# Kernel optimization log

Hardware: AMD Instinct MI355X
Metric: run time of the kernel (lower is better)

The kernel has to match this reference:

```python
import jax, jax.numpy as jnp
import numpy as np
from jax import lax

EPS = 1e-5

def _dsconv(x, dw, pw, g, b, m, v, relu):
    # x: [B,C,H,W]; dw: [C,1,3,3] depthwise; pw: [C,C,1,1] pointwise; eval-mode BN
    C = x.shape[1]
    y = lax.conv_general_dilated(x, dw, (1, 1), 'SAME', feature_group_count=C)
    y = lax.conv_general_dilated(y, pw, (1, 1), 'SAME')
    scale = (g * lax.rsqrt(v + EPS))[None, :, None, None]
    y = y * scale + (b - m * g * lax.rsqrt(v + EPS))[None, :, None, None]
    return jnp.maximum(y, 0.0) if relu else y

def _attention(x, wq, bq, wk, bk, wv, bv, gamma):
    b, c, h, w = x.shape
    n = h * w
    xf = x.reshape(b, c, n)                      # [B,C,N]
    q = jnp.einsum('oc,bcn->bon', wq, xf) + bq[None, :, None]   # [B,C/8,N]
    k = jnp.einsum('oc,bcn->bon', wk, xf) + bk[None, :, None]   # [B,C/8,N]
    v = jnp.einsum('oc,bcn->bon', wv, xf) + bv[None, :, None]   # [B,C,N]
    logits = jnp.einsum('bdm,bdn->bmn', q, k)    # q^T k, [B,N,N]
    attn = jax.nn.softmax(logits, axis=2)
    out = jnp.einsum('bcn,bmn->bcm', v, attn).reshape(b, c, h, w)
    return gamma[0] * out + x

def setup_inputs() -> dict:
    key = jax.random.key(0)
    ks = jax.random.split(key, 20)
    B, C, H, W = 64, 256, 32, 32
    C8 = C // 8
    rn = lambda k, s, sc: (jax.random.normal(k, s, dtype=jnp.float32) * sc)
    return {
        'x': rn(ks[0], (B, C, H, W), 1.0),
        'dw1': rn(ks[1], (C, 1, 3, 3), 0.2),
        'pw1': rn(ks[2], (C, C, 1, 1), 0.06),
        'bn1_g': jax.random.uniform(ks[3], (C,), jnp.float32, 0.5, 1.5),
        'bn1_b': rn(ks[4], (C,), 0.1),
        'bn1_m': rn(ks[5], (C,), 0.1),
        'bn1_v': jax.random.uniform(ks[6], (C,), jnp.float32, 0.5, 1.5),
        'dw2': rn(ks[7], (C, 1, 3, 3), 0.2),
        'pw2': rn(ks[8], (C, C, 1, 1), 0.06),
        'bn2_g': jax.random.uniform(ks[9], (C,), jnp.float32, 0.5, 1.5),
        'bn2_b': rn(ks[10], (C,), 0.1),
        'bn2_m': rn(ks[11], (C,), 0.1),
        'bn2_v': jax.random.uniform(ks[12], (C,), jnp.float32, 0.5, 1.5),
        'wq': rn(ks[13], (C8, C), 0.06),
        'bq': rn(ks[14], (C8,), 0.02),
        'wk': rn(ks[15], (C8, C), 0.06),
        'bk': rn(ks[16], (C8,), 0.02),
        'wv': rn(ks[17], (C, C), 0.06),
        'bv': rn(ks[18], (C,), 0.02),
        'gamma': rn(ks[19], (1,), 0.5),
    }

def reference(x, dw1, pw1, bn1_g, bn1_b, bn1_m, bn1_v,
              dw2, pw2, bn2_g, bn2_b, bn2_m, bn2_v,
              wq, bq, wk, bk, wv, bv, gamma):
    out = _dsconv(x, dw1, pw1, bn1_g, bn1_b, bn1_m, bn1_v, relu=True)
    out = _dsconv(out, dw2, pw2, bn2_g, bn2_b, bn2_m, bn2_v, relu=False)
    out = _attention(out + x, wq, bq, wk, bk, wv, bv, gamma)
    return jnp.maximum(out, 0.0)
```

## Files before the change

kernel.cpp:

```cpp
#include <hip/hip_runtime.h>
#include <cstdint>
#include <cstddef>

#define B_ 64
#define C_ 256
#define N_ 1024

typedef short v8s __attribute__((ext_vector_type(8)));
typedef float v4f __attribute__((ext_vector_type(4)));
typedef unsigned int u32;
typedef unsigned short u16;

__device__ __forceinline__ float bf2f(u16 u) {
  return __uint_as_float(((u32)u) << 16);
}
__device__ __forceinline__ u16 f2bf(float f) {
  u32 x = __float_as_uint(f);
  x += 0x7fffu + ((x >> 16) & 1u);
  return (u16)(x >> 16);
}
__device__ __forceinline__ u32 pack2(float a, float b) {
  return (u32)f2bf(a) | ((u32)f2bf(b) << 16);
}

typedef __attribute__((address_space(3))) unsigned int lds_as_t;
typedef __attribute__((address_space(1))) const unsigned int glb_as_t;
__device__ __forceinline__ void ld_lds16(const u16* g, u16* l) {
  __builtin_amdgcn_global_load_lds((glb_as_t*)g, (lds_as_t*)l, 16, 0, 0);
}

__global__ __launch_bounds__(256) void prep(
    const float* __restrict__ g1, const float* __restrict__ b1,
    const float* __restrict__ m1, const float* __restrict__ v1,
    const float* __restrict__ g2, const float* __restrict__ b2,
    const float* __restrict__ m2, const float* __restrict__ v2,
    const float* __restrict__ wq, const float* __restrict__ bq,
    const float* __restrict__ wk, const float* __restrict__ bk,
    const float* __restrict__ wv, const float* __restrict__ bv,
    const float* __restrict__ pw1, const float* __restrict__ pw2,
    const float* __restrict__ dw1, const float* __restrict__ dw2,
    float* __restrict__ scale1, float* __restrict__ shift1,
    float* __restrict__ scale2, float* __restrict__ shift2,
    float* __restrict__ dwT1, float* __restrict__ dwT2,
    u16* __restrict__ pw1b, u16* __restrict__ pw2b, u16* __restrict__ wcatb,
    float* __restrict__ bcat) {
  const int gt = blockIdx.x * 256 + threadIdx.x;
  if (gt < 256) {
    float s1 = g1[gt] * rsqrtf(v1[gt] + 1e-5f);
    scale1[gt] = s1;
    shift1[gt] = b1[gt] - m1[gt] * s1;
    float s2 = g2[gt] * rsqrtf(v2[gt] + 1e-5f);
    scale2[gt] = s2;
    shift2[gt] = b2[gt] - m2[gt] * s2;
  }
  if (gt < 320) bcat[gt] = (gt < 32) ? bq[gt] : (gt < 64) ? bk[gt - 32] : bv[gt - 64];
  if (gt < 2304) {
    dwT1[(gt % 9) * 256 + gt / 9] = dw1[gt];
    dwT2[(gt % 9) * 256 + gt / 9] = dw2[gt];
  }
  for (int e = gt; e < 65536; e += 16384) {
    pw1b[e] = f2bf(pw1[e]);
    pw2b[e] = f2bf(pw2[e]);
  }
  for (int e = gt; e < 81920; e += 16384) {
    const int o = e >> 8;
    float w = (o < 32) ? wq[e] : (o < 64) ? wk[e - 8192] : wv[e - 16384];
    wcatb[e] = f2bf(w);
  }
}

__global__ __launch_bounds__(256) void transpose_x(const float* __restrict__ x,
                                                   u16* __restrict__ xt) {
  __shared__ float t[64][65];
  const int b = blockIdx.z, c0 = blockIdx.y * 64, n0 = blockIdx.x * 64;
  const float* xp = x + ((size_t)b * C_ + c0) * N_ + n0;
  const int tn = threadIdx.x & 63, tc = threadIdx.x >> 6;
#pragma unroll
  for (int i = 0; i < 16; ++i)
    t[tc + 4 * i][tn] = xp[(size_t)(tc + 4 * i) * N_ + tn];
  __syncthreads();
  u16* op = xt + ((size_t)b * N_ + n0) * C_ + c0;
  const int oc = threadIdx.x & 63, on = threadIdx.x >> 6;
#pragma unroll
  for (int i = 0; i < 16; ++i)
    op[(size_t)(on + 4 * i) * C_ + oc] = f2bf(t[oc][on + 4 * i]);
}

__global__ __launch_bounds__(256) void dw_nhwc(const u16* __restrict__ src,
                                               const float* __restrict__ wT,
                                               u16* __restrict__ dst) {
  __shared__ float wl[9][256];
  const int b = blockIdx.y;
  for (int e = threadIdx.x; e < 2304; e += 256) wl[e >> 8][e & 255] = wT[e];
  __syncthreads();
  const int pl = threadIdx.x >> 5, c0 = (threadIdx.x & 31) * 8;
  const int p = blockIdx.x * 8 + pl;
  const int h = p >> 5, wx = p & 31;
  const u16* sp = src + (size_t)b * N_ * C_;
  float acc[8] = {0.f, 0.f, 0.f, 0.f, 0.f, 0.f, 0.f, 0.f};
#pragma unroll
  for (int dh = -1; dh <= 1; ++dh) {
    const int hh = h + dh;
    if (hh < 0 || hh > 31) continue;
#pragma unroll
    for (int dx = -1; dx <= 1; ++dx) {
      const int ww = wx + dx;
      if (ww < 0 || ww > 31) continue;
      const int k = (dh + 1) * 3 + (dx + 1);
      const uint4 v = *(const uint4*)(sp + (size_t)(hh * 32 + ww) * C_ + c0);
      const u32 vv[4] = {v.x, v.y, v.z, v.w};
#pragma unroll
      for (int j = 0; j < 4; ++j) {
        acc[2 * j] += bf2f((u16)(vv[j] & 0xffffu)) * wl[k][c0 + 2 * j];
        acc[2 * j + 1] += bf2f((u16)(vv[j] >> 16)) * wl[k][c0 + 2 * j + 1];
      }
    }
  }
  uint4 o4;
  o4.x = pack2(acc[0], acc[1]);
  o4.y = pack2(acc[2], acc[3]);
  o4.z = pack2(acc[4], acc[5]);
  o4.w = pack2(acc[6], acc[7]);
  *(uint4*)(dst + ((size_t)b * N_ + p) * C_ + c0) = o4;
}

template <int EPI>
__global__ __launch_bounds__(256) void gemm(
    const u16* __restrict__ X, const u16* __restrict__ W,
    const float* __restrict__ scale, const float* __restrict__ shift,
    const u16* __restrict__ resid, u16* __restrict__ Y, u16* __restrict__ Y2) {
  __shared__ u16 Xs[128][64];
  __shared__ u16 Ws[128][64];
  const int tid = threadIdx.x;
  const int b = blockIdx.z;
  const int n0 = blockIdx.x * 128, o0 = blockIdx.y * 128;
  const int wid = tid >> 6, lane = tid & 63;
  const int wn = wid & 1, wo = wid >> 1;
  const int l15 = lane & 15, l4 = lane >> 4;
  const int lr = lane >> 3, lc = (lane & 7) * 8;

  v4f acc[4][4];
#pragma unroll
  for (int i = 0; i < 4; ++i)
#pragma unroll
    for (int j = 0; j < 4; ++j) acc[i][j] = v4f{0.f, 0.f, 0.f, 0.f};

  for (int k0 = 0; k0 < C_; k0 += 64) {
#pragma unroll
    for (int g = 0; g < 4; ++g) {
      const int base = wid * 32 + g * 8;
      const int xr = n0 + base + lr;
      ld_lds16(X + ((size_t)b * N_ + xr) * C_ + k0 + lc, &Xs[base][0]);
      int wr = o0 + base + lr;
      if (EPI == 2 && wr > 319) wr = 319;
      ld_lds16(W + (size_t)wr * C_ + k0 + lc, &Ws[base][0]);
    }
    __syncthreads();
#pragma unroll
    for (int ks = 0; ks < 2; ++ks) {
      v8s af[4], bf4[4];
#pragma unroll
      for (int f = 0; f < 4; ++f) {
        af[f] = *(const v8s*)&Ws[wo * 64 + f * 16 + l15][ks * 32 + l4 * 8];
        bf4[f] = *(const v8s*)&Xs[wn * 64 + f * 16 + l15][ks * 32 + l4 * 8];
      }
#pragma unroll
      for (int i = 0; i < 4; ++i)
#pragma unroll
        for (int j = 0; j < 4; ++j)
          acc[i][j] = __builtin_amdgcn_mfma_f32_16x16x32_bf16(
              af[i], bf4[j], acc[i][j], 0, 0, 0);
    }
    __syncthreads();
  }

#pragma unroll
  for (int i = 0; i < 4; ++i) {
    const int obase = o0 + wo * 64 + i * 16 + l4 * 4;
#pragma unroll
    for (int j = 0; j < 4; ++j) {
      const int n = n0 + wn * 64 + j * 16 + l15;
      float y0 = acc[i][j][0], y1 = acc[i][j][1];
      float y2 = acc[i][j][2], y3 = acc[i][j][3];
      if constexpr (EPI == 0 || EPI == 1) {
        const float4 sc = *(const float4*)&scale[obase];
        const float4 sh = *(const float4*)&shift[obase];
        y0 = y0 * sc.x + sh.x;
        y1 = y1 * sc.y + sh.y;
        y2 = y2 * sc.z + sh.z;
        y3 = y3 * sc.w + sh.w;
        if constexpr (EPI == 0) {
          y0 = fmaxf(y0, 0.f);
          y1 = fmaxf(y1, 0.f);
          y2 = fmaxf(y2, 0.f);
          y3 = fmaxf(y3, 0.f);
        } else {
          const uint2 rb =
              *(const uint2*)(resid + ((size_t)b * N_ + n) * C_ + obase);
          y0 += bf2f((u16)(rb.x & 0xffffu));
          y1 += bf2f((u16)(rb.x >> 16));
          y2 += bf2f((u16)(rb.y & 0xffffu));
          y3 += bf2f((u16)(rb.y >> 16));
        }
        uint2 st;
        st.x = pack2(y0, y1);
        st.y = pack2(y2, y3);
        *(uint2*)&Y[((size_t)b * N_ + n) * C_ + obase] = st;
      } else {
        if (obase >= 320) continue;
        const float4 bi = *(const float4*)&shift[obase];
        y0 += bi.x;
        y1 += bi.y;
        y2 += bi.z;
        y3 += bi.w;
        if (obase < 64) {
          uint2 st;
          st.x = pack2(y0, y1);
          st.y = pack2(y2, y3);
          *(uint2*)&Y[((size_t)b * N_ + n) * 64 + obase] = st;
        } else {
          const int c = obase - 64;
          Y2[((size_t)b * C_ + c) * N_ + n] = f2bf(y0);
          Y2[((size_t)b * C_ + c + 1) * N_ + n] = f2bf(y1);
          Y2[((size_t)b * C_ + c + 2) * N_ + n] = f2bf(y2);
          Y2[((size_t)b * C_ + c + 3) * N_ + n] = f2bf(y3);
        }
      }
    }
  }
}

__global__ __launch_bounds__(256) void flash(const u16* __restrict__ qk,
                                             const u16* __restrict__ vchw,
                                             const u16* __restrict__ abf,
                                             const float* __restrict__ gamma_p,
                                             float* __restrict__ out) {
  const int b = blockIdx.y;
  const int m0 = blockIdx.x * 64;
  const int tid = threadIdx.x, wid = tid >> 6, lane = tid & 63;
  const int l15 = lane & 15, l4 = lane >> 4;
  const int mw = m0 + wid * 16;

  __shared__ u16 Vs[2][256][64];
  __shared__ u16 Plds[4][16][72];

  const u16* qkb = qk + (size_t)b * N_ * 64;
  const u16* vb = vchw + (size_t)b * C_ * N_;

  const v8s qf = *(const v8s*)&qkb[(size_t)(mw + l15) * 64 + l4 * 8];

  const int src_c = lane >> 3;
  const int src_j = (lane & 7) ^ (lane >> 3);

  v8s kf[4];
#pragma unroll
  for (int g = 0; g < 8; ++g) {
    const int base = wid * 64 + g * 8;
    ld_lds16(vb + (size_t)(base + src_c) * N_ + src_j * 8, &Vs[0][base][0]);
  }
#pragma unroll
  for (int f = 0; f < 4; ++f)
    kf[f] = *(const v8s*)&qkb[(size_t)(f * 16 + l15) * 64 + 32 + l4 * 8];
  __syncthreads();

  float M = -3e38f, S = 0.f;
  v4f acc[16];
#pragma unroll
  for (int i = 0; i < 16; ++i) acc[i] = v4f{0.f, 0.f, 0.f, 0.f};

  for (int t = 0; t < 16; ++t) {
    const int cur = t & 1;
    v4f lt[4];
#pragma unroll
    for (int f = 0; f < 4; ++f)
      lt[f] = __builtin_amdgcn_mfma_f32_16x16x32_bf16(
          kf[f], qf, v4f{0.f, 0.f, 0.f, 0.f}, 0, 0, 0);
    if (t < 15) {
      const int n1 = (t + 1) * 64;
#pragma unroll
      for (int g = 0; g < 8; ++g) {
        const int base = wid * 64 + g * 8;
        ld_lds16(vb + (size_t)(base + src_c) * N_ + n1 + src_j * 8,
                 &Vs[cur ^ 1][base][0]);
      }
#pragma unroll
      for (int f = 0; f < 4; ++f)
        kf[f] = *(const v8s*)&qkb[(size_t)(n1 + f * 16 + l15) * 64 + 32 +
                                  l4 * 8];
    }
    float pmax = -3e38f;
#pragma unroll
    for (int f = 0; f < 4; ++f)
#pragma unroll
      for (int r = 0; r < 4; ++r) pmax = fmaxf(pmax, lt[f][r]);
    pmax = fmaxf(pmax, __shfl_xor(pmax, 16));
    pmax = fmaxf(pmax, __shfl_xor(pmax, 32));
    const float Mnew = fmaxf(M, pmax);
    if (__any(Mnew > M)) {
      const float fsc = __expf(M - Mnew);
      S *= fsc;
      M = Mnew;
      float fr[4];
#pragma unroll
      for (int r = 0; r < 4; ++r) fr[r] = __shfl(fsc, l4 * 4 + r);
#pragma unroll
      for (int cf = 0; cf < 16; ++cf)
#pragma unroll
        for (int r = 0; r < 4; ++r) acc[cf][r] *= fr[r];
    }
    float ssum = 0.f;
#pragma unroll
    for (int f = 0; f < 4; ++f) {
      const float p0 = __expf(lt[f][0] - M);
      const float p1 = __expf(lt[f][1] - M);
      const float p2 = __expf(lt[f][2] - M);
      const float p3 = __expf(lt[f][3] - M);
      ssum += (p0 + p1) + (p2 + p3);
      uint2 pw;
      pw.x = pack2(p0, p1);
      pw.y = pack2(p2, p3);
      *(uint2*)&Plds[wid][l15][f * 16 + l4 * 4] = pw;
    }
    S += ssum;
#pragma unroll
    for (int ks = 0; ks < 2; ++ks) {
      const v8s pa = *(const v8s*)&Plds[wid][l15][ks * 32 + l4 * 8];
#pragma unroll
      for (int cf = 0; cf < 16; ++cf) {
        const int col = 8 * (((ks * 4) + l4) ^ (l15 & 7));
        const v8s vf = *(const v8s*)&Vs[cur][cf * 16 + l15][col];
        acc[cf] = __builtin_amdgcn_mfma_f32_16x16x32_bf16(pa, vf, acc[cf], 0,
                                                          0, 0);
      }
    }
    __syncthreads();
  }

  S += __shfl_xor(S, 16);
  S += __shfl_xor(S, 32);
  const float inv = 1.f / S;
  const float g = gamma_p[0];
  float invr[4];
#pragma unroll
  for (int r = 0; r < 4; ++r) invr[r] = __shfl(inv, l4 * 4 + r);
  const int mb = mw + l4 * 4;
#pragma unroll
  for (int cf = 0; cf < 16; ++cf) {
    const int c = cf * 16 + l15;
    float4 y;
    float* yp = (float*)&y;
#pragma unroll
    for (int r = 0; r < 4; ++r) {
      const float av = bf2f(abf[((size_t)b * N_ + mb + r) * C_ + c]);
      yp[r] = fmaxf(g * acc[cf][r] * invr[r] + av, 0.f);
    }
    *(float4*)&out[((size_t)b * C_ + c) * N_ + mb] = y;
  }
}

extern "C" void kernel_launch(void* const* d_in, const int* in_sizes, int n_in,
                              void* d_out, int out_size, void* d_ws,
                              size_t ws_size, hipStream_t stream) {
  const float* x = (const float*)d_in[0];
  const float* dw1 = (const float*)d_in[1];
  const float* pw1 = (const float*)d_in[2];
  const float* bn1g = (const float*)d_in[3];
  const float* bn1b = (const float*)d_in[4];
  const float* bn1m = (const float*)d_in[5];
  const float* bn1v = (const float*)d_in[6];
  const float* dw2 = (const float*)d_in[7];
  const float* pw2 = (const float*)d_in[8];
  const float* bn2g = (const float*)d_in[9];
  const float* bn2b = (const float*)d_in[10];
  const float* bn2m = (const float*)d_in[11];
  const float* bn2v = (const float*)d_in[12];
  const float* wq = (const float*)d_in[13];
  const float* bq = (const float*)d_in[14];
  const float* wk = (const float*)d_in[15];
  const float* bk = (const float*)d_in[16];
  const float* wv = (const float*)d_in[17];
  const float* bv = (const float*)d_in[18];
  const float* gamma = (const float*)d_in[19];
  float* out = (float*)d_out;

  char* ws = (char*)d_ws;
  size_t off = 0;
  auto alloc = [&](size_t bytes) {
    void* p = ws + off;
    off += (bytes + 255) & ~(size_t)255;
    return p;
  };
  const size_t NE = (size_t)B_ * N_ * C_;

  u16* bufA = (u16*)alloc(NE * 2);
  u16* bufB = (u16*)alloc(NE * 2);
  u16* bufC = (u16*)alloc(NE * 2);
  u16* abf = (u16*)alloc(NE * 2);
  float* scale1 = (float*)alloc(256 * 4);
  float* shift1 = (float*)alloc(256 * 4);
  float* scale2 = (float*)alloc(256 * 4);
  float* shift2 = (float*)alloc(256 * 4);
  float* dwT1 = (float*)alloc(2304 * 4);
  float* dwT2 = (float*)alloc(2304 * 4);
  u16* pw1b = (u16*)alloc(65536 * 2);
  u16* pw2b = (u16*)alloc(65536 * 2);
  u16* wcatb = (u16*)alloc(81920 * 2);
  float* bcat = (float*)alloc(320 * 4);

  u16* xt = bufA;
  u16* t1 = bufB;
  u16* y1 = bufC;
  u16* t2 = bufB;
  u16* qkbuf = bufC;
  u16* vchw = bufA;

  prep<<<64, 256, 0, stream>>>(bn1g, bn1b, bn1m, bn1v, bn2g, bn2b, bn2m, bn2v,
                               wq, bq, wk, bk, wv, bv, pw1, pw2, dw1, dw2,
                               scale1, shift1, scale2, shift2, dwT1, dwT2,
                               pw1b, pw2b, wcatb, bcat);
  transpose_x<<<dim3(16, 4, B_), 256, 0, stream>>>(x, xt);
  dw_nhwc<<<dim3(128, B_), 256, 0, stream>>>(xt, dwT1, t1);
  gemm<0><<<dim3(8, 2, B_), 256, 0, stream>>>(t1, pw1b, scale1, shift1,
                                              nullptr, y1, nullptr);
  dw_nhwc<<<dim3(128, B_), 256, 0, stream>>>(y1, dwT2, t2);
  gemm<1><<<dim3(8, 2, B_), 256, 0, stream>>>(t2, pw2b, scale2, shift2, xt,
                                              abf, nullptr);
  gemm<2><<<dim3(8, 3, B_), 256, 0, stream>>>(abf, wcatb, nullptr, bcat,
                                              nullptr, qkbuf, vchw);
  flash<<<dim3(16, B_), 256, 0, stream>>>(qkbuf, vchw, abf, gamma, out);
}
```

Baseline: 259.6 us.

## Precompute softmax max in a pre-pass, stage GEMM epilogue stores through LDS

```diff
diff --git a/kernel.cpp b/kernel.cpp
--- a/kernel.cpp
+++ b/kernel.cpp
@@ -5,6 +5,7 @@
 #define B_ 64
 #define C_ 256
 #define N_ 1024
+#define LOG2E 1.4426950408889634f
 
 typedef short v8s __attribute__((ext_vector_type(8)));
 typedef float v4f __attribute__((ext_vector_type(4)));
@@ -53,7 +54,9 @@
     scale2[gt] = s2;
     shift2[gt] = b2[gt] - m2[gt] * s2;
   }
-  if (gt < 320) bcat[gt] = (gt < 32) ? bq[gt] : (gt < 64) ? bk[gt - 32] : bv[gt - 64];
+  if (gt < 320)
+    bcat[gt] = (gt < 32) ? bq[gt] * LOG2E
+                         : (gt < 64) ? bk[gt - 32] : bv[gt - 64];
   if (gt < 2304) {
     dwT1[(gt % 9) * 256 + gt / 9] = dw1[gt];
     dwT2[(gt % 9) * 256 + gt / 9] = dw2[gt];
@@ -64,7 +67,8 @@
   }
   for (int e = gt; e < 81920; e += 16384) {
     const int o = e >> 8;
-    float w = (o < 32) ? wq[e] : (o < 64) ? wk[e - 8192] : wv[e - 16384];
+    float w = (o < 32) ? wq[e] * LOG2E
+                       : (o < 64) ? wk[e - 8192] : wv[e - 16384];
     wcatb[e] = f2bf(w);
   }
 }
@@ -129,8 +133,11 @@
     const u16* __restrict__ X, const u16* __restrict__ W,
     const float* __restrict__ scale, const float* __restrict__ shift,
     const u16* __restrict__ resid, u16* __restrict__ Y, u16* __restrict__ Y2) {
-  __shared__ u16 Xs[128][64];
-  __shared__ u16 Ws[128][64];
+  __shared__ u16 smem[17408];
+  u16(*Xs)[64] = (u16(*)[64])smem;
+  u16(*Ws)[64] = (u16(*)[64])(smem + 8192);
+  u16(*Ys)[136] = (u16(*)[136])smem;
+
   const int tid = threadIdx.x;
   const int b = blockIdx.z;
   const int n0 = blockIdx.x * 128, o0 = blockIdx.y * 128;
@@ -149,8 +156,8 @@
 #pragma unroll
     for (int g = 0; g < 4; ++g) {
       const int base = wid * 32 + g * 8;
-      const int xr = n0 + base + lr;
-      ld_lds16(X + ((size_t)b * N_ + xr) * C_ + k0 + lc, &Xs[base][0]);
+      ld_lds16(X + ((size_t)b * N_ + n0 + base + lr) * C_ + k0 + lc,
+               &Xs[base][0]);
       int wr = o0 + base + lr;
       if (EPI == 2 && wr > 319) wr = 319;
       ld_lds16(W + (size_t)wr * C_ + k0 + lc, &Ws[base][0]);
@@ -161,8 +168,13 @@
       v8s af[4], bf4[4];
 #pragma unroll
       for (int f = 0; f < 4; ++f) {
-        af[f] = *(const v8s*)&Ws[wo * 64 + f * 16 + l15][ks * 32 + l4 * 8];
-        bf4[f] = *(const v8s*)&Xs[wn * 64 + f * 16 + l15][ks * 32 + l4 * 8];
+        if constexpr (EPI != 2) {
+          af[f] = *(const v8s*)&Ws[wo * 64 + f * 16 + l15][ks * 32 + l4 * 8];
+          bf4[f] = *(const v8s*)&Xs[wn * 64 + f * 16 + l15][ks * 32 + l4 * 8];
+        } else {
+          af[f] = *(const v8s*)&Xs[wn * 64 + f * 16 + l15][ks * 32 + l4 * 8];
+          bf4[f] = *(const v8s*)&Ws[wo * 64 + f * 16 + l15][ks * 32 + l4 * 8];
+        }
       }
 #pragma unroll
       for (int i = 0; i < 4; ++i)
@@ -174,21 +186,20 @@
     __syncthreads();
   }
 
-#pragma unroll
-  for (int i = 0; i < 4; ++i) {
-    const int obase = o0 + wo * 64 + i * 16 + l4 * 4;
-#pragma unroll
-    for (int j = 0; j < 4; ++j) {
-      const int n = n0 + wn * 64 + j * 16 + l15;
-      float y0 = acc[i][j][0], y1 = acc[i][j][1];
-      float y2 = acc[i][j][2], y3 = acc[i][j][3];
-      if constexpr (EPI == 0 || EPI == 1) {
-        const float4 sc = *(const float4*)&scale[obase];
-        const float4 sh = *(const float4*)&shift[obase];
-        y0 = y0 * sc.x + sh.x;
-        y1 = y1 * sc.y + sh.y;
-        y2 = y2 * sc.z + sh.z;
-        y3 = y3 * sc.w + sh.w;
+  if constexpr (EPI != 2) {
+#pragma unroll
+    for (int i = 0; i < 4; ++i) {
+      const int oL = wo * 64 + i * 16 + l4 * 4;
+      const int o = o0 + oL;
+      const float4 sc = *(const float4*)&scale[o];
+      const float4 sh = *(const float4*)&shift[o];
+#pragma unroll
+      for (int j = 0; j < 4; ++j) {
+        const int nL = wn * 64 + j * 16 + l15;
+        float y0 = acc[i][j][0] * sc.x + sh.x;
+        float y1 = acc[i][j][1] * sc.y + sh.y;
+        float y2 = acc[i][j][2] * sc.z + sh.z;
+        float y3 = acc[i][j][3] * sc.w + sh.w;
         if constexpr (EPI == 0) {
           y0 = fmaxf(y0, 0.f);
           y1 = fmaxf(y1, 0.f);
@@ -196,7 +207,7 @@
           y3 = fmaxf(y3, 0.f);
         } else {
           const uint2 rb =
-              *(const uint2*)(resid + ((size_t)b * N_ + n) * C_ + obase);
+              *(const uint2*)(resid + ((size_t)b * N_ + n0 + nL) * C_ + o);
           y0 += bf2f((u16)(rb.x & 0xffffu));
           y1 += bf2f((u16)(rb.x >> 16));
           y2 += bf2f((u16)(rb.y & 0xffffu));
@@ -205,26 +216,59 @@
         uint2 st;
         st.x = pack2(y0, y1);
         st.y = pack2(y2, y3);
-        *(uint2*)&Y[((size_t)b * N_ + n) * C_ + obase] = st;
-      } else {
-        if (obase >= 320) continue;
-        const float4 bi = *(const float4*)&shift[obase];
-        y0 += bi.x;
-        y1 += bi.y;
-        y2 += bi.z;
-        y3 += bi.w;
-        if (obase < 64) {
+        *(uint2*)&Ys[nL][oL] = st;
+      }
+    }
+    __syncthreads();
+#pragma unroll
+    for (int s = 0; s < 8; ++s) {
+      const int nL = s * 16 + (tid >> 4);
+      const int slot = tid & 15;
+      const uint4 v = *(const uint4*)&Ys[nL][slot * 8];
+      *(uint4*)&Y[((size_t)b * N_ + n0 + nL) * C_ + o0 + slot * 8] = v;
+    }
+  } else {
+    float bj[4];
+#pragma unroll
+    for (int j = 0; j < 4; ++j) {
+      int o = o0 + wo * 64 + j * 16 + l15;
+      bj[j] = shift[o > 319 ? 319 : o];
+    }
+    if (o0 == 0 && wo == 0) {
+#pragma unroll
+      for (int i = 0; i < 4; ++i) {
+        const int nB = n0 + wn * 64 + i * 16 + l4 * 4;
+#pragma unroll
+        for (int j = 0; j < 4; ++j) {
+          const int o = j * 16 + l15;
+#pragma unroll
+          for (int r = 0; r < 4; ++r)
+            Y[((size_t)b * N_ + nB + r) * 64 + o] = f2bf(acc[i][j][r] + bj[j]);
+        }
+      }
+    } else {
+#pragma unroll
+      for (int i = 0; i < 4; ++i) {
+        const int nL = wn * 64 + i * 16 + l4 * 4;
+#pragma unroll
+        for (int j = 0; j < 4; ++j) {
+          const int oL = wo * 64 + j * 16 + l15;
           uint2 st;
-          st.x = pack2(y0, y1);
-          st.y = pack2(y2, y3);
-          *(uint2*)&Y[((size_t)b * N_ + n) * 64 + obase] = st;
-        } else {
-          const int c = obase - 64;
-          Y2[((size_t)b * C_ + c) * N_ + n] = f2bf(y0);
-          Y2[((size_t)b * C_ + c + 1) * N_ + n] = f2bf(y1);
-          Y2[((size_t)b * C_ + c + 2) * N_ + n] = f2bf(y2);
-          Y2[((size_t)b * C_ + c + 3) * N_ + n] = f2bf(y3);
+          st.x = pack2(acc[i][j][0] + bj[j], acc[i][j][1] + bj[j]);
+          st.y = pack2(acc[i][j][2] + bj[j], acc[i][j][3] + bj[j]);
+          *(uint2*)&Ys[oL][nL] = st;
         }
+      }
+    }
+    __syncthreads();
+#pragma unroll
+    for (int s = 0; s < 8; ++s) {
+      const int oL = s * 16 + (tid >> 4);
+      const int c = o0 + oL - 64;
+      if (c >= 0 && c < 256) {
+        const int slot = tid & 15;
+        const uint4 v = *(const uint4*)&Ys[oL][slot * 8];
+        *(uint4*)&Y2[((size_t)b * C_ + c) * N_ + n0 + slot * 8] = v;
       }
     }
   }
@@ -235,8 +279,8 @@
                                              const u16* __restrict__ abf,
                                              const float* __restrict__ gamma_p,
                                              float* __restrict__ out) {
-  const int b = blockIdx.y;
-  const int m0 = blockIdx.x * 64;
+  const int b = blockIdx.x;
+  const int m0 = blockIdx.y * 64;
   const int tid = threadIdx.x, wid = tid >> 6, lane = tid & 63;
   const int l15 = lane & 15, l4 = lane >> 4;
   const int mw = m0 + wid * 16;
@@ -246,27 +290,54 @@
 
   const u16* qkb = qk + (size_t)b * N_ * 64;
   const u16* vb = vchw + (size_t)b * C_ * N_;
-
   const v8s qf = *(const v8s*)&qkb[(size_t)(mw + l15) * 64 + l4 * 8];
 
   const int src_c = lane >> 3;
   const int src_j = (lane & 7) ^ (lane >> 3);
 
-  v8s kf[4];
 #pragma unroll
   for (int g = 0; g < 8; ++g) {
     const int base = wid * 64 + g * 8;
     ld_lds16(vb + (size_t)(base + src_c) * N_ + src_j * 8, &Vs[0][base][0]);
   }
+
+  float Mloc = -3e38f;
+  v8s kf[4];
+#pragma unroll
+  for (int f = 0; f < 4; ++f)
+    kf[f] = *(const v8s*)&qkb[(size_t)(f * 16 + l15) * 64 + 32 + l4 * 8];
+  for (int t = 0; t < 16; ++t) {
+    v8s kn[4];
+    if (t < 15) {
+      const int n1 = (t + 1) * 64;
+#pragma unroll
+      for (int f = 0; f < 4; ++f)
+        kn[f] =
+            *(const v8s*)&qkb[(size_t)(n1 + f * 16 + l15) * 64 + 32 + l4 * 8];
+    }
+#pragma unroll
+    for (int f = 0; f < 4; ++f) {
+      const v4f lt = __builtin_amdgcn_mfma_f32_16x16x32_bf16(
+          kf[f], qf, v4f{0.f, 0.f, 0.f, 0.f}, 0, 0, 0);
+      Mloc = fmaxf(Mloc, fmaxf(fmaxf(lt[0], lt[1]), fmaxf(lt[2], lt[3])));
+    }
+    if (t < 15) {
+#pragma unroll
+      for (int f = 0; f < 4; ++f) kf[f] = kn[f];
+    }
+  }
+  Mloc = fmaxf(Mloc, __shfl_xor(Mloc, 16));
+  Mloc = fmaxf(Mloc, __shfl_xor(Mloc, 32));
+  const float M = Mloc;
+
+  v4f acc[16];
+#pragma unroll
+  for (int i = 0; i < 16; ++i) acc[i] = v4f{0.f, 0.f, 0.f, 0.f};
+  float S0 = 0.f, S1 = 0.f, S2 = 0.f, S3 = 0.f;
 #pragma unroll
   for (int f = 0; f < 4; ++f)
     kf[f] = *(const v8s*)&qkb[(size_t)(f * 16 + l15) * 64 + 32 + l4 * 8];
   __syncthreads();
-
-  float M = -3e38f, S = 0.f;
-  v4f acc[16];
-#pragma unroll
-  for (int i = 0; i < 16; ++i) acc[i] = v4f{0.f, 0.f, 0.f, 0.f};
 
   for (int t = 0; t < 16; ++t) {
     const int cur = t & 1;
@@ -285,43 +356,25 @@
       }
 #pragma unroll
       for (int f = 0; f < 4; ++f)
-        kf[f] = *(const v8s*)&qkb[(size_t)(n1 + f * 16 + l15) * 64 + 32 +
-                                  l4 * 8];
-    }
-    float pmax = -3e38f;
-#pragma unroll
-    for (int f = 0; f < 4; ++f)
-#pragma unroll
-      for (int r = 0; r < 4; ++r) pmax = fmaxf(pmax, lt[f][r]);
-    pmax = fmaxf(pmax, __shfl_xor(pmax, 16));
-    pmax = fmaxf(pmax, __shfl_xor(pmax, 32));
-    const float Mnew = fmaxf(M, pmax);
-    if (__any(Mnew > M)) {
-      const float fsc = __expf(M - Mnew);
-      S *= fsc;
-      M = Mnew;
-      float fr[4];
-#pragma unroll
-      for (int r = 0; r < 4; ++r) fr[r] = __shfl(fsc, l4 * 4 + r);
-#pragma unroll
-      for (int cf = 0; cf < 16; ++cf)
-#pragma unroll
-        for (int r = 0; r < 4; ++r) acc[cf][r] *= fr[r];
-    }
-    float ssum = 0.f;
+        kf[f] =
+            *(const v8s*)&qkb[(size_t)(n1 + f * 16 + l15) * 64 + 32 + l4 * 8];
+    }
 #pragma unroll
     for (int f = 0; f < 4; ++f) {
-      const float p0 = __expf(lt[f][0] - M);
-      const float p1 = __expf(lt[f][1] - M);
-      const float p2 = __expf(lt[f][2] - M);
-      const float p3 = __expf(lt[f][3] - M);
-      ssum += (p0 + p1) + (p2 + p3);
+      const float p0 = exp2f(lt[f][0] - M);
+      const float p1 = exp2f(lt[f][1] - M);
+      const float p2 = exp2f(lt[f][2] - M);
+      const float p3 = exp2f(lt[f][3] - M);
+      S0 += p0;
+      S1 += p1;
+      S2 += p2;
+      S3 += p3;
       uint2 pw;
       pw.x = pack2(p0, p1);
       pw.y = pack2(p2, p3);
       *(uint2*)&Plds[wid][l15][f * 16 + l4 * 4] = pw;
     }
-    S += ssum;
+    __builtin_amdgcn_s_setprio(1);
 #pragma unroll
     for (int ks = 0; ks < 2; ++ks) {
       const v8s pa = *(const v8s*)&Plds[wid][l15][ks * 32 + l4 * 8];
@@ -333,9 +386,11 @@
                                                           0, 0);
       }
     }
+    __builtin_amdgcn_s_setprio(0);
     __syncthreads();
   }
 
+  float S = (S0 + S1) + (S2 + S3);
   S += __shfl_xor(S, 16);
   S += __shfl_xor(S, 32);
   const float inv = 1.f / S;
@@ -405,7 +460,7 @@
   u16* pw1b = (u16*)alloc(65536 * 2);
   u16* pw2b = (u16*)alloc(65536 * 2);
   u16* wcatb = (u16*)alloc(81920 * 2);
-  float* bcat = (float*)alloc(320 * 4);
+  float* bcat = (float*)alloc(384 * 4);
 
   u16* xt = bufA;
   u16* t1 = bufB;
@@ -427,5 +482,5 @@
                                               abf, nullptr);
   gemm<2><<<dim3(8, 3, B_), 256, 0, stream>>>(abf, wcatb, nullptr, bcat,
                                               nullptr, qkbuf, vchw);
-  flash<<<dim3(16, B_), 256, 0, stream>>>(qkbuf, vchw, abf, gamma, out);
-}
+  flash<<<dim3(64, 16), 256, 0, stream>>>(qkbuf, vchw, abf, gamma, out);
+}
```

Result: no change. 258.2 us (-0.6%).
